# Optimization experiments

Hardware: AMD Instinct MI355X
Metric: run time of the kernel (lower is better)

Reference implementation:

```python
import jax, jax.numpy as jnp
import numpy as np


def setup_inputs() -> dict:
    key = jax.random.key(0)
    k1, k2 = jax.random.split(key)
    B, M, N = 16, 4096, 4096
    target_points = jax.random.normal(k1, (B, M, 2), dtype=jnp.float32)
    actual_points = jax.random.normal(k2, (B, N, 2), dtype=jnp.float32)
    return {"target_points": target_points, "actual_points": actual_points}


def reference(target_points, actual_points):
    # target_points: [B, M, 2], actual_points: [B, N, 2]
    # diff[b, m, n] = || target[b, m] - actual[b, n] ||_2
    d = target_points[:, :, None, :] - actual_points[:, None, :, :]  # [B, M, N, 2]
    diff = jnp.sqrt(jnp.sum(d * d, axis=-1))  # [B, M, N]
    forward_loss = jnp.min(diff, axis=2)   # [B, M] nearest actual for each target
    backward_loss = jnp.min(diff, axis=1)  # [B, N] nearest target for each actual
    return (forward_loss, backward_loss)
```

## Files before the change

kernel.cpp:

```cpp
#include <hip/hip_runtime.h>
#include <math.h>


typedef float f32x2 __attribute__((ext_vector_type(2)));

#define BLK 256
#define TM  8
#define RC  32

__device__ __forceinline__ float min3f(float a, float b, float c) {
    float d;
    asm("v_min3_f32 %0, %1, %2, %3" : "=v"(d) : "v"(a), "v"(b), "v"(c));
    return d;
}

__global__ __launch_bounds__(256) void chamfer_init(unsigned int* __restrict__ out, int n) {
    int i = blockIdx.x * 256 + threadIdx.x;
    if (i < n) out[i] = 0x7F800000u;
}

__global__ __launch_bounds__(BLK) void chamfer_partial(
    const float2* __restrict__ tpts,
    const float2* __restrict__ apts,
    unsigned int* __restrict__ out,
    int M, int N, int B)
{
    const int b   = blockIdx.y;
    const int zc  = blockIdx.z;
    const int dir = zc & 1;
    const int rc  = zc >> 1;

    const float2* __restrict__ Q = dir ? apts : tpts;
    const float2* __restrict__ R = dir ? tpts : apts;
    const int NQ = dir ? N : M;
    const int NR = dir ? M : N;
    unsigned int* __restrict__ o =
        out + (dir ? ((size_t)B * M + (size_t)b * N) : ((size_t)b * M));

    const float2* __restrict__ q = Q + (size_t)b * NQ;
    const float2* __restrict__ r = R + (size_t)b * NR;

    const int clen = (NR + RC - 1) / RC;
    const int rbeg = rc * clen;
    const int rend = (rbeg + clen < NR) ? (rbeg + clen) : NR;
    if (rbeg >= rend) return;

    int   qi[TM];
    float n2x[TM], n2y[TM], qn[TM], mn[TM];
#pragma unroll
    for (int k = 0; k < TM; ++k) {
        qi[k] = blockIdx.x * (BLK * TM) + k * BLK + (int)threadIdx.x;
        int idx = qi[k] < NQ ? qi[k] : NQ - 1;
        float2 p = q[idx];
        n2x[k] = -2.0f * p.x;
        n2y[k] = -2.0f * p.y;
        qn[k]  = fmaf(p.y, p.y, p.x * p.x);
        mn[k]  = 3.0e38f;
    }

    int n = rbeg;
    for (; n < rend && (n & 1); ++n) {
        float2 p = r[n];
        float va = fmaf(p.y, p.y, p.x * p.x);
#pragma unroll
        for (int k = 0; k < TM; ++k) {
            float v = fmaf(n2x[k], p.x, fmaf(n2y[k], p.y, va));
            mn[k] = fminf(mn[k], v);
        }
    }

    for (; n + 8 <= rend; n += 8) {
        f32x2 px[4], py[4], va[4];
#pragma unroll
        for (int g = 0; g < 4; ++g) {
            float4 p4 = *(const float4*)&r[n + 2 * g];
            px[g] = (f32x2){p4.x, p4.z};
            py[g] = (f32x2){p4.y, p4.w};
            va[g] = __builtin_elementwise_fma(py[g], py[g], px[g] * px[g]);
        }
#pragma unroll
        for (int k = 0; k < TM; ++k) {
            f32x2 cx = (f32x2)(n2x[k]);
            f32x2 cy = (f32x2)(n2y[k]);
            f32x2 v0 = __builtin_elementwise_fma(cx, px[0],
                        __builtin_elementwise_fma(cy, py[0], va[0]));
            f32x2 v1 = __builtin_elementwise_fma(cx, px[1],
                        __builtin_elementwise_fma(cy, py[1], va[1]));
            f32x2 v2 = __builtin_elementwise_fma(cx, px[2],
                        __builtin_elementwise_fma(cy, py[2], va[2]));
            f32x2 v3 = __builtin_elementwise_fma(cx, px[3],
                        __builtin_elementwise_fma(cy, py[3], va[3]));
            float m = min3f(v0.x, v0.y, v1.x);
            m       = min3f(m, v1.y, v2.x);
            m       = min3f(m, v2.y, v3.x);
            mn[k]   = min3f(m, v3.y, mn[k]);
        }
    }

    for (; n < rend; ++n) {
        float2 p = r[n];
        float va = fmaf(p.y, p.y, p.x * p.x);
#pragma unroll
        for (int k = 0; k < TM; ++k) {
            float v = fmaf(n2x[k], p.x, fmaf(n2y[k], p.y, va));
            mn[k] = fminf(mn[k], v);
        }
    }

#pragma unroll
    for (int k = 0; k < TM; ++k) {
        if (qi[k] < NQ) {
            float d2 = fmaxf(mn[k] + qn[k], 0.0f);
            atomicMin(&o[qi[k]], __float_as_uint(d2));
        }
    }
}

__global__ __launch_bounds__(256) void chamfer_sqrt(
    unsigned int* __restrict__ io, int n)
{
    int i = blockIdx.x * 256 + threadIdx.x;
    if (i < n) {
        float d2 = __uint_as_float(io[i]);
        ((float*)io)[i] = sqrtf(d2);
    }
}

extern "C" void kernel_launch(void* const* d_in, const int* in_sizes, int n_in,
                              void* d_out, int out_size, void* d_ws, size_t ws_size,
                              hipStream_t stream) {
    const float2* tpts = (const float2*)d_in[0];
    const float2* apts = (const float2*)d_in[1];
    unsigned int* out = (unsigned int*)d_out;

    const int B = 16;
    const int M = in_sizes[0] / (B * 2);
    const int N = in_sizes[1] / (B * 2);
    const int total = B * (M + N);

    chamfer_init<<<(total + 255) / 256, 256, 0, stream>>>(out, total);

    const int maxQ = M > N ? M : N;
    dim3 grid((maxQ + BLK * TM - 1) / (BLK * TM), B, 2 * RC);
    chamfer_partial<<<grid, dim3(BLK), 0, stream>>>(tpts, apts, out, M, N, B);

    chamfer_sqrt<<<(total + 255) / 256, 256, 0, stream>>>(out, total);
}
```

Baseline: 40.66 us.

## Transpose reference points to SoA workspace for vectorized x/y loads

Adds a pre-pass kernel that rewrites both point sets into a structure-of-arrays layout in the workspace. The main kernel then loads x and y as separate float4 vectors, so no shuffling is needed to form packed f32x2 operands. It also hoists the splatted query coefficients into f32x2 registers and adds a min-blocks hint to launch_bounds. The extra launch and workspace traffic are the cost, and a plain AoS fallback kernel runs when the workspace is too small.

```diff
diff --git a/kernel.cpp b/kernel.cpp
--- a/kernel.cpp
+++ b/kernel.cpp
@@ -19,11 +19,28 @@
     if (i < n) out[i] = 0x7F800000u;
 }
 
-__global__ __launch_bounds__(BLK) void chamfer_partial(
+__global__ __launch_bounds__(256) void chamfer_soa(
+    const float2* __restrict__ tpts, const float2* __restrict__ apts,
+    float* __restrict__ ws, int M, int N, int B, int S)
+{
+    int idx = blockIdx.x * 256 + threadIdx.x;
+    int total = B * (M + N);
+    if (idx >= total) return;
+    int set, b, n;
+    float2 p;
+    if (idx < B * M) { set = 0; b = idx / M; n = idx % M; p = tpts[idx]; }
+    else { int j = idx - B * M; set = 1; b = j / N; n = j % N; p = apts[j]; }
+    float* base = ws + ((size_t)set * B + b) * (2 * (size_t)S);
+    base[n] = p.x;
+    base[S + n] = p.y;
+}
+
+__global__ __launch_bounds__(BLK, 4) void chamfer_partial(
     const float2* __restrict__ tpts,
     const float2* __restrict__ apts,
+    const float* __restrict__ soa,
     unsigned int* __restrict__ out,
-    int M, int N, int B)
+    int M, int N, int B, int S)
 {
     const int b   = blockIdx.y;
     const int zc  = blockIdx.z;
@@ -31,14 +48,15 @@
     const int rc  = zc >> 1;
 
     const float2* __restrict__ Q = dir ? apts : tpts;
-    const float2* __restrict__ R = dir ? tpts : apts;
     const int NQ = dir ? N : M;
     const int NR = dir ? M : N;
+    const int rsel = 1 - dir;
     unsigned int* __restrict__ o =
         out + (dir ? ((size_t)B * M + (size_t)b * N) : ((size_t)b * M));
 
     const float2* __restrict__ q = Q + (size_t)b * NQ;
-    const float2* __restrict__ r = R + (size_t)b * NR;
+    const float*  __restrict__ RX = soa + ((size_t)rsel * B + b) * (2 * (size_t)S);
+    const float*  __restrict__ RY = RX + S;
 
     const int clen = (NR + RC - 1) / RC;
     const int rbeg = rc * clen;
@@ -46,63 +64,55 @@
     if (rbeg >= rend) return;
 
     int   qi[TM];
-    float n2x[TM], n2y[TM], qn[TM], mn[TM];
+    float qn[TM], mn[TM];
+    f32x2 cx[TM], cy[TM];
 #pragma unroll
     for (int k = 0; k < TM; ++k) {
         qi[k] = blockIdx.x * (BLK * TM) + k * BLK + (int)threadIdx.x;
         int idx = qi[k] < NQ ? qi[k] : NQ - 1;
         float2 p = q[idx];
-        n2x[k] = -2.0f * p.x;
-        n2y[k] = -2.0f * p.y;
-        qn[k]  = fmaf(p.y, p.y, p.x * p.x);
-        mn[k]  = 3.0e38f;
+        cx[k] = (f32x2)(-2.0f * p.x);
+        cy[k] = (f32x2)(-2.0f * p.y);
+        qn[k] = fmaf(p.y, p.y, p.x * p.x);
+        mn[k] = 3.0e38f;
     }
 
     int n = rbeg;
-    for (; n < rend && (n & 1); ++n) {
-        float2 p = r[n];
-        float va = fmaf(p.y, p.y, p.x * p.x);
+    for (; n + 8 <= rend; n += 8) {
+        float4 xa = *(const float4*)&RX[n];
+        float4 xb = *(const float4*)&RX[n + 4];
+        float4 ya = *(const float4*)&RY[n];
+        float4 yb = *(const float4*)&RY[n + 4];
+        f32x2 px0 = (f32x2){xa.x, xa.y}, px1 = (f32x2){xa.z, xa.w};
+        f32x2 px2 = (f32x2){xb.x, xb.y}, px3 = (f32x2){xb.z, xb.w};
+        f32x2 py0 = (f32x2){ya.x, ya.y}, py1 = (f32x2){ya.z, ya.w};
+        f32x2 py2 = (f32x2){yb.x, yb.y}, py3 = (f32x2){yb.z, yb.w};
+        f32x2 va0 = __builtin_elementwise_fma(py0, py0, px0 * px0);
+        f32x2 va1 = __builtin_elementwise_fma(py1, py1, px1 * px1);
+        f32x2 va2 = __builtin_elementwise_fma(py2, py2, px2 * px2);
+        f32x2 va3 = __builtin_elementwise_fma(py3, py3, px3 * px3);
 #pragma unroll
         for (int k = 0; k < TM; ++k) {
-            float v = fmaf(n2x[k], p.x, fmaf(n2y[k], p.y, va));
-            mn[k] = fminf(mn[k], v);
-        }
-    }
-
-    for (; n + 8 <= rend; n += 8) {
-        f32x2 px[4], py[4], va[4];
-#pragma unroll
-        for (int g = 0; g < 4; ++g) {
-            float4 p4 = *(const float4*)&r[n + 2 * g];
-            px[g] = (f32x2){p4.x, p4.z};
-            py[g] = (f32x2){p4.y, p4.w};
-            va[g] = __builtin_elementwise_fma(py[g], py[g], px[g] * px[g]);
-        }
-#pragma unroll
-        for (int k = 0; k < TM; ++k) {
-            f32x2 cx = (f32x2)(n2x[k]);
-            f32x2 cy = (f32x2)(n2y[k]);
-            f32x2 v0 = __builtin_elementwise_fma(cx, px[0],
-                        __builtin_elementwise_fma(cy, py[0], va[0]));
-            f32x2 v1 = __builtin_elementwise_fma(cx, px[1],
-                        __builtin_elementwise_fma(cy, py[1], va[1]));
-            f32x2 v2 = __builtin_elementwise_fma(cx, px[2],
-                        __builtin_elementwise_fma(cy, py[2], va[2]));
-            f32x2 v3 = __builtin_elementwise_fma(cx, px[3],
-                        __builtin_elementwise_fma(cy, py[3], va[3]));
+            f32x2 v0 = __builtin_elementwise_fma(cx[k], px0,
+                        __builtin_elementwise_fma(cy[k], py0, va0));
+            f32x2 v1 = __builtin_elementwise_fma(cx[k], px1,
+                        __builtin_elementwise_fma(cy[k], py1, va1));
+            f32x2 v2 = __builtin_elementwise_fma(cx[k], px2,
+                        __builtin_elementwise_fma(cy[k], py2, va2));
+            f32x2 v3 = __builtin_elementwise_fma(cx[k], px3,
+                        __builtin_elementwise_fma(cy[k], py3, va3));
             float m = min3f(v0.x, v0.y, v1.x);
             m       = min3f(m, v1.y, v2.x);
             m       = min3f(m, v2.y, v3.x);
             mn[k]   = min3f(m, v3.y, mn[k]);
         }
     }
-
     for (; n < rend; ++n) {
-        float2 p = r[n];
-        float va = fmaf(p.y, p.y, p.x * p.x);
+        float x = RX[n], y = RY[n];
+        float va = fmaf(y, y, x * x);
 #pragma unroll
         for (int k = 0; k < TM; ++k) {
-            float v = fmaf(n2x[k], p.x, fmaf(n2y[k], p.y, va));
+            float v = fmaf(cx[k].x, x, fmaf(cy[k].x, y, va));
             mn[k] = fminf(mn[k], v);
         }
     }
@@ -116,14 +126,48 @@
     }
 }
 
-__global__ __launch_bounds__(256) void chamfer_sqrt(
-    unsigned int* __restrict__ io, int n)
+__global__ __launch_bounds__(256) void chamfer_sqrt(unsigned int* __restrict__ io, int n) {
+    int i = blockIdx.x * 256 + threadIdx.x;
+    if (i < n) ((float*)io)[i] = sqrtf(__uint_as_float(io[i]));
+}
+
+__global__ __launch_bounds__(BLK) void chamfer_partial_aos(
+    const float2* __restrict__ tpts, const float2* __restrict__ apts,
+    unsigned int* __restrict__ out, int M, int N, int B)
 {
-    int i = blockIdx.x * 256 + threadIdx.x;
-    if (i < n) {
-        float d2 = __uint_as_float(io[i]);
-        ((float*)io)[i] = sqrtf(d2);
-    }
+    const int b = blockIdx.y, zc = blockIdx.z;
+    const int dir = zc & 1, rc = zc >> 1;
+    const float2* __restrict__ Q = dir ? apts : tpts;
+    const float2* __restrict__ R = dir ? tpts : apts;
+    const int NQ = dir ? N : M, NR = dir ? M : N;
+    unsigned int* __restrict__ o =
+        out + (dir ? ((size_t)B * M + (size_t)b * N) : ((size_t)b * M));
+    const float2* __restrict__ q = Q + (size_t)b * NQ;
+    const float2* __restrict__ r = R + (size_t)b * NR;
+    const int clen = (NR + RC - 1) / RC;
+    const int rbeg = rc * clen;
+    const int rend = (rbeg + clen < NR) ? (rbeg + clen) : NR;
+    if (rbeg >= rend) return;
+    int qi[TM]; float n2x[TM], n2y[TM], qn[TM], mn[TM];
+#pragma unroll
+    for (int k = 0; k < TM; ++k) {
+        qi[k] = blockIdx.x * (BLK * TM) + k * BLK + (int)threadIdx.x;
+        int idx = qi[k] < NQ ? qi[k] : NQ - 1;
+        float2 p = q[idx];
+        n2x[k] = -2.0f * p.x; n2y[k] = -2.0f * p.y;
+        qn[k] = fmaf(p.y, p.y, p.x * p.x); mn[k] = 3.0e38f;
+    }
+    for (int n = rbeg; n < rend; ++n) {
+        float2 p = r[n];
+        float va = fmaf(p.y, p.y, p.x * p.x);
+#pragma unroll
+        for (int k = 0; k < TM; ++k)
+            mn[k] = fminf(mn[k], fmaf(n2x[k], p.x, fmaf(n2y[k], p.y, va)));
+    }
+#pragma unroll
+    for (int k = 0; k < TM; ++k)
+        if (qi[k] < NQ)
+            atomicMin(&o[qi[k]], __float_as_uint(fmaxf(mn[k] + qn[k], 0.0f)));
 }
 
 extern "C" void kernel_launch(void* const* d_in, const int* in_sizes, int n_in,
@@ -136,13 +180,24 @@
     const int B = 16;
     const int M = in_sizes[0] / (B * 2);
     const int N = in_sizes[1] / (B * 2);
+    const int S = M > N ? M : N;
     const int total = B * (M + N);
 
     chamfer_init<<<(total + 255) / 256, 256, 0, stream>>>(out, total);
 
-    const int maxQ = M > N ? M : N;
-    dim3 grid((maxQ + BLK * TM - 1) / (BLK * TM), B, 2 * RC);
-    chamfer_partial<<<grid, dim3(BLK), 0, stream>>>(tpts, apts, out, M, N, B);
+    size_t soa_bytes = (size_t)2 * B * 2 * S * sizeof(float);
+    dim3 grid((S + BLK * TM - 1) / (BLK * TM), B, 2 * RC);
+
+    if (ws_size >= soa_bytes) {
+        float* soa = (float*)d_ws;
+        chamfer_soa<<<(total + 255) / 256, 256, 0, stream>>>(
+            tpts, apts, soa, M, N, B, S);
+        chamfer_partial<<<grid, dim3(BLK), 0, stream>>>(
+            tpts, apts, soa, out, M, N, B, S);
+    } else {
+        chamfer_partial_aos<<<grid, dim3(BLK), 0, stream>>>(
+            tpts, apts, out, M, N, B);
+    }
 
     chamfer_sqrt<<<(total + 255) / 256, 256, 0, stream>>>(out, total);
 }
```

Measured after the change: 42.81 us. 5.3% more time.
